# Performance work log

Measured on AMD Instinct MI355X. Metric: run time of the kernel, lower is better.

## Reference

```python
import jax, jax.numpy as jnp
import numpy as np

N, D = 8192, 128


def setup_inputs() -> dict:
    key = jax.random.key(0)
    k1, k2 = jax.random.split(key)
    z1 = jax.random.normal(k1, (N, D), dtype=jnp.float32)
    z2 = jax.random.normal(k2, (N, D), dtype=jnp.float32)
    return {"z1": z1, "z2": z2}


def reference(z1, z2):
    # logits[i, j] = -||z1_i - z2_j||^2, computed via the cdist-as-GEMM identity
    # (same math as dz = z2[None,:,:] - z1[:,None,:]; -einsum('...d,...d->...', dz, dz))
    sq1 = jnp.sum(z1 * z1, axis=-1)  # [N]
    sq2 = jnp.sum(z2 * z2, axis=-1)  # [N]
    logits = 2.0 * (z1 @ z2.T) - sq1[:, None] - sq2[None, :]  # [N, N]
    # CrossEntropyLoss with labels = arange(N): mean over rows of -log_softmax diag
    logp = jax.nn.log_softmax(logits, axis=-1)
    return -jnp.mean(jnp.diagonal(logp))
```

## Files before the change

kernel.cpp:

```cpp
#include <hip/hip_runtime.h>
#include <hip/hip_bf16.h>

typedef unsigned int   u32;
typedef unsigned short u16;

#define NN   8192
#define DD   128
#define CCH  32
#define CHUNK (NN / CCH)
#define JT   64
#define NT   (CHUNK / JT)
#define NIB  (NN / 256)

#define LOG2E 1.4426950408889634f
#define LN2F  0.6931471805599453f
#define BIAS  32.0f

typedef __bf16 bf16x8 __attribute__((ext_vector_type(8)));
typedef float  f32x16 __attribute__((ext_vector_type(16)));
typedef float  f32x2  __attribute__((ext_vector_type(2)));

__device__ __forceinline__ u16 f2bf(float x) {
    u32 u = __float_as_uint(x);
    u += 0x7fffu + ((u >> 16) & 1u);
    return (u16)(u >> 16);
}

__global__ __launch_bounds__(256) void prep_kernel(
    const float* __restrict__ z1, const float* __restrict__ z2,
    u32* __restrict__ b1, u32* __restrict__ b2,
    float* __restrict__ negsq2b, float* __restrict__ diag)
{
    int row  = blockIdx.x * 4 + (threadIdx.x >> 6);
    int lane = threadIdx.x & 63;
    float2 a = reinterpret_cast<const float2*>(z1)[row * 64 + lane];
    float2 b = reinterpret_cast<const float2*>(z2)[row * 64 + lane];
    b1[row * 64 + lane] = (u32)f2bf(a.x) | ((u32)f2bf(a.y) << 16);
    b2[row * 64 + lane] = (u32)f2bf(b.x) | ((u32)f2bf(b.y) << 16);
    float dot = a.x * b.x + a.y * b.y;
    float sq  = b.x * b.x + b.y * b.y;
    #pragma unroll
    for (int o = 32; o > 0; o >>= 1) {
        dot += __shfl_xor(dot, o);
        sq  += __shfl_xor(sq, o);
    }
    if (lane == 0) {
        negsq2b[row] = -sq * LOG2E - BIAS;
        diag[row]    = 2.0f * dot - sq;
    }
}

__global__ __launch_bounds__(256, 2) void score_kernel(
    const u16* __restrict__ b1, const u16* __restrict__ b2,
    const float* __restrict__ negsq2b, float* __restrict__ partS)
{
    __shared__ alignas(16) u16 tile[2][JT * DD];
    __shared__ alignas(16) float nqs[CHUNK];
    const int tid  = threadIdx.x;
    const int lane = tid & 63;
    const int wid  = tid >> 6;
    const int r    = lane & 31, hi = lane >> 5;

    const int f     = blockIdx.x;
    const int chunk = (f >> 3) & 31;
    const int iblk  = (f & 7) * 4 + (f >> 8);
    const int j0    = chunk * CHUNK;
    const int i0w   = iblk * 256 + wid * 64;

    bf16x8 zf0[8], zf1[8];
    #pragma unroll
    for (int kk = 0; kk < 8; ++kk) {
        zf0[kk] = *reinterpret_cast<const bf16x8*>(b1 + (size_t)(i0w + r)      * DD + kk * 16 + hi * 8);
        zf1[kk] = *reinterpret_cast<const bf16x8*>(b1 + (size_t)(i0w + 32 + r) * DD + kk * 16 + hi * 8);
    }
    nqs[tid] = negsq2b[j0 + tid];

    const int sl   = lane & 15;
    const int rrow = lane >> 4;

    auto stage = [&](int t, int buf) {
        #pragma unroll
        for (int u = 0; u < 4; ++u) {
            int row   = wid * 16 + u * 4 + rrow;
            int gslot = sl ^ (row & 15);
            const u16* src = b2 + (size_t)(j0 + t * JT + row) * DD + gslot * 8;
            u16* dst = &tile[buf][(wid * 16 + u * 4) * DD];
            __builtin_amdgcn_global_load_lds(
                (const __attribute__((address_space(1))) void*)src,
                (__attribute__((address_space(3))) void*)dst, 16, 0, 0);
        }
    };

    float s0 = 0.f, s1 = 0.f, s2 = 0.f, s3 = 0.f;
    const f32x2 C2v = {2.0f * LOG2E, 2.0f * LOG2E};
    const int sw = r & 15;

    int cur = 0;
    stage(0, 0);
    for (int t = 0; t < NT; ++t) {
        __syncthreads();
        if (t + 1 < NT) stage(t + 1, cur ^ 1);
        const u16* tp = tile[cur];
        #pragma unroll
        for (int jj = 0; jj < 2; ++jj) {
            const float* nqb = &nqs[t * JT + jj * 32 + 4 * hi];
            float4 nq0 = *reinterpret_cast<const float4*>(nqb);
            float4 nq1 = *reinterpret_cast<const float4*>(nqb + 8);
            float4 nq2 = *reinterpret_cast<const float4*>(nqb + 16);
            float4 nq3 = *reinterpret_cast<const float4*>(nqb + 24);
            bf16x8 av[8];
            #pragma unroll
            for (int kk = 0; kk < 8; ++kk) {
                int off = (jj * 32 + r) * DD + (((2 * kk + hi) ^ sw) << 3);
                av[kk] = *reinterpret_cast<const bf16x8*>(tp + off);
            }
            f32x16 acc0 = {0.f}; f32x16 acc1 = {0.f};
            #pragma unroll
            for (int kk = 0; kk < 8; ++kk) {
                acc0 = __builtin_amdgcn_mfma_f32_32x32x16_bf16(av[kk], zf0[kk], acc0, 0, 0, 0);
                acc1 = __builtin_amdgcn_mfma_f32_32x32x16_bf16(av[kk], zf1[kk], acc1, 0, 0, 0);
            }
            const float nqa[16] = {nq0.x, nq0.y, nq0.z, nq0.w,
                                   nq1.x, nq1.y, nq1.z, nq1.w,
                                   nq2.x, nq2.y, nq2.z, nq2.w,
                                   nq3.x, nq3.y, nq3.z, nq3.w};
            #pragma unroll
            for (int q = 0; q < 8; ++q) {
                f32x2 n2 = {nqa[2 * q], nqa[2 * q + 1]};
                f32x2 a0 = {acc0[2 * q], acc0[2 * q + 1]};
                f32x2 t0 = a0 * C2v + n2;
                s0 += __builtin_amdgcn_exp2f(t0.x);
                s1 += __builtin_amdgcn_exp2f(t0.y);
                f32x2 a1 = {acc1[2 * q], acc1[2 * q + 1]};
                f32x2 t1 = a1 * C2v + n2;
                s2 += __builtin_amdgcn_exp2f(t1.x);
                s3 += __builtin_amdgcn_exp2f(t1.y);
            }
        }
        cur ^= 1;
    }

    float sum0 = s0 + s1, sum1 = s2 + s3;
    sum0 += __shfl_xor(sum0, 32);
    sum1 += __shfl_xor(sum1, 32);
    if (hi == 0) {
        partS[(size_t)chunk * NN + i0w + r]      = sum0;
        partS[(size_t)chunk * NN + i0w + 32 + r] = sum1;
    }
}

__global__ __launch_bounds__(256) void finalize1_kernel(
    const float* __restrict__ partS, const float* __restrict__ diag,
    float* __restrict__ blocksum)
{
    __shared__ float red[4];
    int r = blockIdx.x * 256 + threadIdx.x;
    float s = 0.f;
    #pragma unroll
    for (int c = 0; c < CCH; ++c) s += partS[(size_t)c * NN + r];
    float lse = (BIAS + __builtin_amdgcn_logf(s)) * LN2F;
    float acc = lse - diag[r];
    #pragma unroll
    for (int o = 32; o > 0; o >>= 1) acc += __shfl_xor(acc, o);
    int lane = threadIdx.x & 63, wid = threadIdx.x >> 6;
    if (lane == 0) red[wid] = acc;
    __syncthreads();
    if (threadIdx.x == 0)
        blocksum[blockIdx.x] = red[0] + red[1] + red[2] + red[3];
}

__global__ void finalize2_kernel(const float* __restrict__ blocksum, float* __restrict__ out)
{
    int lane = threadIdx.x;
    float v = (lane < 32) ? blocksum[lane] : 0.f;
    #pragma unroll
    for (int o = 32; o > 0; o >>= 1) v += __shfl_xor(v, o);
    if (lane == 0) out[0] = v * (1.0f / (float)NN);
}

extern "C" void kernel_launch(void* const* d_in, const int* in_sizes, int n_in,
                              void* d_out, int out_size, void* d_ws, size_t ws_size,
                              hipStream_t stream)
{
    const float* z1 = (const float*)d_in[0];
    const float* z2 = (const float*)d_in[1];
    char* ws = (char*)d_ws;

    const size_t bf_bytes = (size_t)NN * DD * 2;
    u32*   b1       = (u32*)ws;
    u32*   b2       = (u32*)(ws + bf_bytes);
    float* negsq2b  = (float*)(ws + 2 * bf_bytes);
    float* diag     = (float*)(ws + 2 * bf_bytes + (size_t)NN * 4);
    float* partS    = (float*)(ws + 2 * bf_bytes + (size_t)NN * 8);
    float* blocksum = (float*)(ws + 2 * bf_bytes + (size_t)NN * 8 + (size_t)CCH * NN * 4);
    float* out      = (float*)d_out;

    prep_kernel<<<NN / 4, 256, 0, stream>>>(z1, z2, b1, b2, negsq2b, diag);
    score_kernel<<<CCH * NIB, 256, 0, stream>>>((const u16*)b1, (const u16*)b2, negsq2b, partS);
    finalize1_kernel<<<NN / 256, 256, 0, stream>>>(partS, diag, blocksum);
    finalize2_kernel<<<1, 64, 0, stream>>>(blocksum, out);
}
```

Baseline: 39.03 us.

## Load z2 operand fragments directly from global memory instead of LDS double-buffering

```diff
diff --git a/kernel.cpp b/kernel.cpp
--- a/kernel.cpp
+++ b/kernel.cpp
@@ -8,8 +8,7 @@
 #define DD   128
 #define CCH  32
 #define CHUNK (NN / CCH)
-#define JT   64
-#define NT   (CHUNK / JT)
+#define NTJ  (CHUNK / 32)
 #define NIB  (NN / 256)
 
 #define LOG2E 1.4426950408889634f
@@ -50,11 +49,10 @@
     }
 }
 
-__global__ __launch_bounds__(256, 2) void score_kernel(
+__global__ __launch_bounds__(256) void score_kernel(
     const u16* __restrict__ b1, const u16* __restrict__ b2,
     const float* __restrict__ negsq2b, float* __restrict__ partS)
 {
-    __shared__ alignas(16) u16 tile[2][JT * DD];
     __shared__ alignas(16) float nqs[CHUNK];
     const int tid  = threadIdx.x;
     const int lane = tid & 63;
@@ -74,73 +72,50 @@
         zf1[kk] = *reinterpret_cast<const bf16x8*>(b1 + (size_t)(i0w + 32 + r) * DD + kk * 16 + hi * 8);
     }
     nqs[tid] = negsq2b[j0 + tid];
+    __syncthreads();
 
-    const int sl   = lane & 15;
-    const int rrow = lane >> 4;
+    f32x2 sA0 = {0.f, 0.f}, sA1 = {0.f, 0.f}, sB0 = {0.f, 0.f}, sB1 = {0.f, 0.f};
+    const f32x2 c2 = {2.0f * LOG2E, 2.0f * LOG2E};
 
-    auto stage = [&](int t, int buf) {
+    #pragma unroll 2
+    for (int t = 0; t < NTJ; ++t) {
+        const u16* bp = b2 + (size_t)(j0 + t * 32 + r) * DD + hi * 8;
+        bf16x8 av[8];
         #pragma unroll
-        for (int u = 0; u < 4; ++u) {
-            int row   = wid * 16 + u * 4 + rrow;
-            int gslot = sl ^ (row & 15);
-            const u16* src = b2 + (size_t)(j0 + t * JT + row) * DD + gslot * 8;
-            u16* dst = &tile[buf][(wid * 16 + u * 4) * DD];
-            __builtin_amdgcn_global_load_lds(
-                (const __attribute__((address_space(1))) void*)src,
-                (__attribute__((address_space(3))) void*)dst, 16, 0, 0);
+        for (int kk = 0; kk < 8; ++kk)
+            av[kk] = *reinterpret_cast<const bf16x8*>(bp + kk * 16);
+
+        f32x16 acc0 = {0.f}; f32x16 acc1 = {0.f};
+        #pragma unroll
+        for (int kk = 0; kk < 8; ++kk) {
+            acc0 = __builtin_amdgcn_mfma_f32_32x32x16_bf16(av[kk], zf0[kk], acc0, 0, 0, 0);
+            acc1 = __builtin_amdgcn_mfma_f32_32x32x16_bf16(av[kk], zf1[kk], acc1, 0, 0, 0);
         }
-    };
 
-    float s0 = 0.f, s1 = 0.f, s2 = 0.f, s3 = 0.f;
-    const f32x2 C2v = {2.0f * LOG2E, 2.0f * LOG2E};
-    const int sw = r & 15;
-
-    int cur = 0;
-    stage(0, 0);
-    for (int t = 0; t < NT; ++t) {
-        __syncthreads();
-        if (t + 1 < NT) stage(t + 1, cur ^ 1);
-        const u16* tp = tile[cur];
+        const float* nqb = &nqs[t * 32 + 4 * hi];
+        float4 nq0 = *reinterpret_cast<const float4*>(nqb);
+        float4 nq1 = *reinterpret_cast<const float4*>(nqb + 8);
+        float4 nq2 = *reinterpret_cast<const float4*>(nqb + 16);
+        float4 nq3 = *reinterpret_cast<const float4*>(nqb + 24);
+        const float4 nqm[4] = {nq0, nq1, nq2, nq3};
         #pragma unroll
-        for (int jj = 0; jj < 2; ++jj) {
-            const float* nqb = &nqs[t * JT + jj * 32 + 4 * hi];
-            float4 nq0 = *reinterpret_cast<const float4*>(nqb);
-            float4 nq1 = *reinterpret_cast<const float4*>(nqb + 8);
-            float4 nq2 = *reinterpret_cast<const float4*>(nqb + 16);
-            float4 nq3 = *reinterpret_cast<const float4*>(nqb + 24);
-            bf16x8 av[8];
-            #pragma unroll
-            for (int kk = 0; kk < 8; ++kk) {
-                int off = (jj * 32 + r) * DD + (((2 * kk + hi) ^ sw) << 3);
-                av[kk] = *reinterpret_cast<const bf16x8*>(tp + off);
-            }
-            f32x16 acc0 = {0.f}; f32x16 acc1 = {0.f};
-            #pragma unroll
-            for (int kk = 0; kk < 8; ++kk) {
-                acc0 = __builtin_amdgcn_mfma_f32_32x32x16_bf16(av[kk], zf0[kk], acc0, 0, 0, 0);
-                acc1 = __builtin_amdgcn_mfma_f32_32x32x16_bf16(av[kk], zf1[kk], acc1, 0, 0, 0);
-            }
-            const float nqa[16] = {nq0.x, nq0.y, nq0.z, nq0.w,
-                                   nq1.x, nq1.y, nq1.z, nq1.w,
-                                   nq2.x, nq2.y, nq2.z, nq2.w,
-                                   nq3.x, nq3.y, nq3.z, nq3.w};
-            #pragma unroll
-            for (int q = 0; q < 8; ++q) {
-                f32x2 n2 = {nqa[2 * q], nqa[2 * q + 1]};
-                f32x2 a0 = {acc0[2 * q], acc0[2 * q + 1]};
-                f32x2 t0 = a0 * C2v + n2;
-                s0 += __builtin_amdgcn_exp2f(t0.x);
-                s1 += __builtin_amdgcn_exp2f(t0.y);
-                f32x2 a1 = {acc1[2 * q], acc1[2 * q + 1]};
-                f32x2 t1 = a1 * C2v + n2;
-                s2 += __builtin_amdgcn_exp2f(t1.x);
-                s3 += __builtin_amdgcn_exp2f(t1.y);
-            }
+        for (int m = 0; m < 4; ++m) {
+            f32x2 n01 = {nqm[m].x, nqm[m].y}, n23 = {nqm[m].z, nqm[m].w};
+            f32x2 a01 = {acc0[4*m],   acc0[4*m+1]}, a23 = {acc0[4*m+2], acc0[4*m+3]};
+            f32x2 t01 = a01 * c2 + n01, t23 = a23 * c2 + n23;
+            f32x2 e01 = {__builtin_amdgcn_exp2f(t01.x), __builtin_amdgcn_exp2f(t01.y)};
+            f32x2 e23 = {__builtin_amdgcn_exp2f(t23.x), __builtin_amdgcn_exp2f(t23.y)};
+            sA0 += e01; sA1 += e23;
+            f32x2 b01 = {acc1[4*m],   acc1[4*m+1]}, b23 = {acc1[4*m+2], acc1[4*m+3]};
+            f32x2 u01 = b01 * c2 + n01, u23 = b23 * c2 + n23;
+            f32x2 f01 = {__builtin_amdgcn_exp2f(u01.x), __builtin_amdgcn_exp2f(u01.y)};
+            f32x2 f23 = {__builtin_amdgcn_exp2f(u23.x), __builtin_amdgcn_exp2f(u23.y)};
+            sB0 += f01; sB1 += f23;
         }
-        cur ^= 1;
     }
 
-    float sum0 = s0 + s1, sum1 = s2 + s3;
+    float sum0 = (sA0.x + sA0.y) + (sA1.x + sA1.y);
+    float sum1 = (sB0.x + sB0.y) + (sB1.x + sB1.y);
     sum0 += __shfl_xor(sum0, 32);
     sum1 += __shfl_xor(sum1, 32);
     if (hi == 0) {
```

New measurement: 52.26 us. 33.9% more time.

## Triple-buffer score tiles with explicit vmcnt waits and fuse final reduction

Applied to the files above, without the earlier changes.

```diff
diff --git a/kernel.cpp b/kernel.cpp
--- a/kernel.cpp
+++ b/kernel.cpp
@@ -29,8 +29,9 @@
 __global__ __launch_bounds__(256) void prep_kernel(
     const float* __restrict__ z1, const float* __restrict__ z2,
     u32* __restrict__ b1, u32* __restrict__ b2,
-    float* __restrict__ negsq2b, float* __restrict__ diag)
-{
+    float* __restrict__ negsq2b, float* __restrict__ diag, u32* __restrict__ ctrl)
+{
+    if (blockIdx.x == 0 && threadIdx.x == 0) ctrl[0] = 0;
     int row  = blockIdx.x * 4 + (threadIdx.x >> 6);
     int lane = threadIdx.x & 63;
     float2 a = reinterpret_cast<const float2*>(z1)[row * 64 + lane];
@@ -50,11 +51,11 @@
     }
 }
 
-__global__ __launch_bounds__(256, 2) void score_kernel(
+__global__ __launch_bounds__(256) void score_kernel(
     const u16* __restrict__ b1, const u16* __restrict__ b2,
     const float* __restrict__ negsq2b, float* __restrict__ partS)
 {
-    __shared__ alignas(16) u16 tile[2][JT * DD];
+    __shared__ alignas(16) u16 tile[3][JT * DD];
     __shared__ alignas(16) float nqs[CHUNK];
     const int tid  = threadIdx.x;
     const int lane = tid & 63;
@@ -74,33 +75,39 @@
         zf1[kk] = *reinterpret_cast<const bf16x8*>(b1 + (size_t)(i0w + 32 + r) * DD + kk * 16 + hi * 8);
     }
     nqs[tid] = negsq2b[j0 + tid];
+    __syncthreads();
 
     const int sl   = lane & 15;
     const int rrow = lane >> 4;
 
-    auto stage = [&](int t, int buf) {
+    auto stage = [&](int t, u16* dst_base) {
         #pragma unroll
         for (int u = 0; u < 4; ++u) {
             int row   = wid * 16 + u * 4 + rrow;
             int gslot = sl ^ (row & 15);
             const u16* src = b2 + (size_t)(j0 + t * JT + row) * DD + gslot * 8;
-            u16* dst = &tile[buf][(wid * 16 + u * 4) * DD];
             __builtin_amdgcn_global_load_lds(
                 (const __attribute__((address_space(1))) void*)src,
-                (__attribute__((address_space(3))) void*)dst, 16, 0, 0);
+                (__attribute__((address_space(3))) void*)(dst_base + (wid * 16 + u * 4) * DD),
+                16, 0, 0);
         }
     };
+
+    stage(0, tile[0]);
+    stage(1, tile[1]);
 
     float s0 = 0.f, s1 = 0.f, s2 = 0.f, s3 = 0.f;
     const f32x2 C2v = {2.0f * LOG2E, 2.0f * LOG2E};
     const int sw = r & 15;
 
-    int cur = 0;
-    stage(0, 0);
+    #pragma unroll
     for (int t = 0; t < NT; ++t) {
-        __syncthreads();
-        if (t + 1 < NT) stage(t + 1, cur ^ 1);
-        const u16* tp = tile[cur];
+        if (t < NT - 1) asm volatile("s_waitcnt vmcnt(4)" ::: "memory");
+        else            asm volatile("s_waitcnt vmcnt(0)" ::: "memory");
+        __builtin_amdgcn_s_barrier();
+        __builtin_amdgcn_sched_barrier(0);
+        if (t + 2 < NT) stage(t + 2, tile[(t + 2) % 3]);
+        const u16* tp = tile[t % 3];
         #pragma unroll
         for (int jj = 0; jj < 2; ++jj) {
             const float* nqb = &nqs[t * JT + jj * 32 + 4 * hi];
@@ -115,11 +122,13 @@
                 av[kk] = *reinterpret_cast<const bf16x8*>(tp + off);
             }
             f32x16 acc0 = {0.f}; f32x16 acc1 = {0.f};
+            __builtin_amdgcn_s_setprio(1);
             #pragma unroll
             for (int kk = 0; kk < 8; ++kk) {
                 acc0 = __builtin_amdgcn_mfma_f32_32x32x16_bf16(av[kk], zf0[kk], acc0, 0, 0, 0);
                 acc1 = __builtin_amdgcn_mfma_f32_32x32x16_bf16(av[kk], zf1[kk], acc1, 0, 0, 0);
             }
+            __builtin_amdgcn_s_setprio(0);
             const float nqa[16] = {nq0.x, nq0.y, nq0.z, nq0.w,
                                    nq1.x, nq1.y, nq1.z, nq1.w,
                                    nq2.x, nq2.y, nq2.z, nq2.w,
@@ -137,7 +146,6 @@
                 s3 += __builtin_amdgcn_exp2f(t1.y);
             }
         }
-        cur ^= 1;
     }
 
     float sum0 = s0 + s1, sum1 = s2 + s3;
@@ -151,9 +159,10 @@
 
 __global__ __launch_bounds__(256) void finalize1_kernel(
     const float* __restrict__ partS, const float* __restrict__ diag,
-    float* __restrict__ blocksum)
+    float* __restrict__ blocksum, u32* __restrict__ ctrl, float* __restrict__ out)
 {
     __shared__ float red[4];
+    __shared__ u32 ticket;
     int r = blockIdx.x * 256 + threadIdx.x;
     float s = 0.f;
     #pragma unroll
@@ -165,17 +174,19 @@
     int lane = threadIdx.x & 63, wid = threadIdx.x >> 6;
     if (lane == 0) red[wid] = acc;
     __syncthreads();
-    if (threadIdx.x == 0)
+    if (threadIdx.x == 0) {
         blocksum[blockIdx.x] = red[0] + red[1] + red[2] + red[3];
-}
-
-__global__ void finalize2_kernel(const float* __restrict__ blocksum, float* __restrict__ out)
-{
-    int lane = threadIdx.x;
-    float v = (lane < 32) ? blocksum[lane] : 0.f;
-    #pragma unroll
-    for (int o = 32; o > 0; o >>= 1) v += __shfl_xor(v, o);
-    if (lane == 0) out[0] = v * (1.0f / (float)NN);
+        __threadfence();
+        ticket = atomicAdd(ctrl, 1u);
+    }
+    __syncthreads();
+    if (ticket == NIB - 1 && threadIdx.x == 0) {
+        __threadfence();
+        float v = 0.f;
+        #pragma unroll
+        for (int c = 0; c < NIB; ++c) v += blocksum[c];
+        out[0] = v * (1.0f / (float)NN);
+    }
 }
 
 extern "C" void kernel_launch(void* const* d_in, const int* in_sizes, int n_in,
@@ -193,10 +204,10 @@
     float* diag     = (float*)(ws + 2 * bf_bytes + (size_t)NN * 4);
     float* partS    = (float*)(ws + 2 * bf_bytes + (size_t)NN * 8);
     float* blocksum = (float*)(ws + 2 * bf_bytes + (size_t)NN * 8 + (size_t)CCH * NN * 4);
+    u32*   ctrl     = (u32*)(ws + 2 * bf_bytes + (size_t)NN * 8 + (size_t)CCH * NN * 4 + 256);
     float* out      = (float*)d_out;
 
-    prep_kernel<<<NN / 4, 256, 0, stream>>>(z1, z2, b1, b2, negsq2b, diag);
+    prep_kernel<<<NN / 4, 256, 0, stream>>>(z1, z2, b1, b2, negsq2b, diag, ctrl);
     score_kernel<<<CCH * NIB, 256, 0, stream>>>((const u16*)b1, (const u16*)b2, negsq2b, partS);
-    finalize1_kernel<<<NN / 256, 256, 0, stream>>>(partS, diag, blocksum);
-    finalize2_kernel<<<1, 64, 0, stream>>>(blocksum, out);
-}
+    finalize1_kernel<<<NIB, 256, 0, stream>>>(partS, diag, blocksum, ctrl, out);
+}
```

Measured after the change: 39.15 us. Within noise of the previous version (+0.3%).
